# Kernel tuning notes

Hardware: AMD Instinct MI355X
Metric: run time of the kernel (lower is better)

## Reference

```python
import jax, jax.numpy as jnp
import numpy as np

RHO = 1.0
L = 50
RS = np.array([20, 40, 80, 160], dtype=np.int32)

def _get_index():
    S = []
    for m in range(-L // 2, L // 2 + 1):
        for n in range(-L // 2, L // 2 + 1):
            if abs(m * n) <= RHO * L // 2:
                S.append((m, n))
    return np.array(S, dtype=np.int32)

IDX = _get_index()          # [449, 2] (m, n) pairs
K = IDX.shape[0]            # 449
B, N, M = 8, 65536, 2       # batch, sequence length, Nmodes (dual-pol)


def setup_inputs() -> dict:
    key = jax.random.key(0)
    ks = jax.random.split(key, 8)
    shp = (B, N, M)
    inp = {
        "E_real": jax.random.normal(ks[0], shp, jnp.float32),
        "E_imag": jax.random.normal(ks[1], shp, jnp.float32),
        "F_real": jax.random.normal(ks[2], shp, jnp.float32),
        "F_imag": jax.random.normal(ks[3], shp, jnp.float32),
        "C1_real": jax.random.normal(ks[4], (len(RS), K), jnp.float32) * 0.01,
        "C1_imag": jax.random.normal(ks[5], (len(RS), K), jnp.float32) * 0.01,
        "C2_real": jax.random.normal(ks[6], (len(RS), K), jnp.float32) * 0.01,
        "C2_imag": jax.random.normal(ks[7], (len(RS), K), jnp.float32) * 0.01,
    }
    # task_info columns: (P [dBm], Fi, Fs [Hz], Nch); Fs must be 2e9 * some Rs entry
    ti = np.zeros((B, 4), dtype=np.float32)
    ti[:, 0] = 2.0
    ti[:, 2] = RS[np.arange(B) % len(RS)].astype(np.float32) * 2e9
    inp["task_info"] = jnp.asarray(ti)
    return inp


def _forward(E_real, E_imag, F_real, F_imag, C1_real, C1_imag, C2_real, C2_imag, task_info):
    E = E_real + 1j * E_imag    # [B, N, M] complex64
    F = F_real + 1j * F_imag

    # choose_C: map Fs -> row of C tables (sorted-Rs order, as in the torch code)
    rs_sorted = jnp.sort(jnp.asarray(RS))
    x = (task_info[:, 2] / 2e9).astype(jnp.int32)              # [B]
    ind = jnp.argmax(x[:, None] == rs_sorted[None, :], axis=-1)  # [B]
    C1 = (C1_real + 1j * C1_imag)[ind]                         # [B, K]
    C2 = (C2_real + 1j * C2_imag)[ind]                         # [B, K]

    ms = jnp.asarray(IDX[:, 0])
    ns = jnp.asarray(IDX[:, 1])

    def step(acc, xs):
        m, n, c1, c2 = xs                                       # c1, c2: [B]
        En  = jnp.roll(E, n, axis=-2)
        Em  = jnp.roll(E, m, axis=-2)
        Emn = jnp.roll(E, m + n, axis=-2)
        Fn  = jnp.roll(F, n, axis=-2)
        Fmn = jnp.roll(F, m + n, axis=-2)
        A = En * jnp.conj(Fmn) * c1[:, None, None] + Fn * jnp.conj(Emn) * c2[:, None, None]
        # (A + A.roll(1, dim=-1)) swaps/combines the two polarizations
        return acc + (A + jnp.roll(A, 1, axis=-1)) * Em, None

    acc, _ = jax.lax.scan(step, jnp.zeros_like(E), (ms, ns, C1.T, C2.T))

    P = jnp.power(10.0, task_info[:, 0] / 10.0) / E.shape[-1]   # [B]
    Eo = F + (jnp.sqrt(P) ** 3)[:, None, None] * acc
    return E[:, L:-L, :], Eo[:, L:-L, :]


def reference(E_real, E_imag, F_real, F_imag, C1_real, C1_imag, C2_real, C2_imag, task_info):
    return _forward(E_real, E_imag, F_real, F_imag,
                    C1_real, C1_imag, C2_real, C2_imag, task_info)
```

## Files before the change

### kernel.cpp

```cpp
#include <hip/hip_runtime.h>
#include <hip/hip_bf16.h>


namespace {

constexpr int NSEQ    = 65536;
constexpr int BATCH   = 8;
constexpr int KTAPS   = 449;
constexpr int NM      = 25;
constexpr int THREADS = 256;
constexpr int TILE    = 512;
constexpr int WIN     = TILE + 4 * NM;
constexpr int GHW     = TILE + 2 * NM;
constexpr int GHH     = (GHW + 1) / 2;

typedef float v2f __attribute__((ext_vector_type(2)));

__device__ inline v2f pkfma(float s, v2f v, v2f acc) {
  return __builtin_elementwise_fma((v2f){s, s}, v, acc);
}

__device__ inline void mac(v2f& U13, v2f& U42, v2f& V13, v2f& V42,
                           const float4 c, const float4 g) {
  const v2f glo = (v2f){g.x, g.y}, ghi = (v2f){g.z, g.w};
  U13 = pkfma(c.x, glo, U13); U42 = pkfma(c.y, glo, U42);
  V13 = pkfma(c.z, ghi, V13); V42 = pkfma(c.w, ghi, V42);
}

__device__ inline unsigned short f2bf(float f) {
  __hip_bfloat16 h = __float2bfloat16(f);
  union { __hip_bfloat16 hh; unsigned short u; } cv;
  cv.hh = h;
  return cv.u;
}

__global__ void prep_c_kernel(const float* __restrict__ c1r, const float* __restrict__ c1i,
                              const float* __restrict__ c2r, const float* __restrict__ c2i,
                              float4* __restrict__ cw) {
  int idx = blockIdx.x * blockDim.x + threadIdx.x;
  if (idx < 4 * KTAPS) cw[idx] = make_float4(c1r[idx], c1i[idx], c2r[idx], c2i[idx]);
}

__device__ inline float4 gh_entry(const float4 e, const float4 f,
                                  const float4 fm, const float4 em) {
  v2f G = (v2f){fm.w * e.w, fm.w * (-e.z)};
  G = pkfma(fm.x, (v2f){e.x, e.y}, G);
  G = pkfma(fm.y, (v2f){e.y, -e.x}, G);
  G = pkfma(fm.z, (v2f){e.z, e.w}, G);
  v2f H = (v2f){em.w * f.w, em.w * (-f.z)};
  H = pkfma(em.x, (v2f){f.x, f.y}, H);
  H = pkfma(em.y, (v2f){f.y, -f.x}, H);
  H = pkfma(em.z, (v2f){f.z, f.w}, H);
  return make_float4(G.x, G.y, H.x, H.y);
}

__global__ __launch_bounds__(THREADS, 4) void hpbc_kernel(
    const float2* __restrict__ er, const float2* __restrict__ ei,
    const float2* __restrict__ fr, const float2* __restrict__ fi,
    const float*  __restrict__ task, const float4* __restrict__ cw,
    unsigned short* __restrict__ out, int nout, int lpad, int ntiles)
{
  __shared__ float4 sE[WIN];
  __shared__ float4 sF[WIN];
  __shared__ float4 ghE[2][GHH];
  __shared__ float4 ghO[2][GHH];

  const int bx   = blockIdx.x;
  const int b    = bx / ntiles;
  const int tile = bx - b * ntiles;
  const int tid  = threadIdx.x;
  const int i0   = lpad + tile * TILE;
  const int elo  = i0 - 2 * NM;

  const float2* erb = er + (size_t)b * NSEQ;
  const float2* eib = ei + (size_t)b * NSEQ;
  const float2* frb = fr + (size_t)b * NSEQ;
  const float2* fib = fi + (size_t)b * NSEQ;

  for (int u = tid; u < WIN; u += THREADS) {
    int g = (elo + u) & (NSEQ - 1);
    float2 a = erb[g], c = eib[g];
    sE[u] = make_float4(a.x, c.x, a.y, c.y);
    float2 d = frb[g], e = fib[g];
    sF[u] = make_float4(d.x, e.x, d.y, e.y);
  }

  const float dbm = task[b * 4 + 0];
  const float fsr = task[b * 4 + 2];
  const int   x   = (int)(fsr / 2.0e9f);
  const int ind = (x == 40) ? 1 : (x == 80) ? 2 : (x == 160) ? 3 : 0;
  const float4* __restrict__ crow = cw + ind * KTAPS;
  const float P  = powf(10.0f, dbm * 0.1f) * 0.5f;
  const float pf = P * sqrtf(P);

  __syncthreads();

  const float4 e0 = sE[tid + NM],            f0 = sF[tid + NM];
  const float4 e1 = sE[tid + THREADS + NM],  f1 = sF[tid + THREADS + NM];
  const bool  has3 = (tid < GHW - 2 * THREADS);
  float4 e2 = make_float4(0,0,0,0), f2 = e2;
  if (has3) { e2 = sE[tid + 2*THREADS + NM]; f2 = sF[tid + 2*THREADS + NM]; }

  v2f A0 = {0,0}, A1 = {0,0}, B0 = {0,0}, B1 = {0,0};
  int kbase = 0, p = 0;
  float4 ebCarry = sE[2*tid + 1 + 2*NM + NM];

  for (int mm = -NM; mm <= NM; ++mm) {
    {
      const int s = NM - mm;
      const float4 g0 = gh_entry(e0, f0, sF[tid + s], sE[tid + s]);
      if (tid & 1) ghO[p][tid >> 1] = g0; else ghE[p][tid >> 1] = g0;
      const float4 g1 = gh_entry(e1, f1, sF[tid + THREADS + s], sE[tid + THREADS + s]);
      if (tid & 1) ghO[p][(tid + THREADS) >> 1] = g1; else ghE[p][(tid + THREADS) >> 1] = g1;
      if (has3) {
        const float4 g2 = gh_entry(e2, f2, sF[tid + 2*THREADS + s], sE[tid + 2*THREADS + s]);
        if (tid & 1) ghO[p][(tid + 2*THREADS) >> 1] = g2; else ghE[p][(tid + 2*THREADS) >> 1] = g2;
      }
    }
    __syncthreads();

    const int am   = mm < 0 ? -mm : mm;
    const int nmax = (mm == 0) ? NM : (NM / am);
    const int q    = nmax & 1;
    const float4* __restrict__ hiArr = q ? ghO[p] : ghE[p];
    const float4* __restrict__ loArr = q ? ghE[p] : ghO[p];
    const int h0 = tid + ((26 + nmax) >> 1);
    const int h1 = tid + ((25 + nmax) >> 1);

    v2f aU13={0,0}, aU42={0,0}, aV13={0,0}, aV42={0,0};
    v2f bU13={0,0}, bU42={0,0}, bV13={0,0}, bV42={0,0};
    float4 cOdd;
    {
      const float4 hi = hiArr[h0], lo = loArr[h1];
      const float4 c0 = crow[kbase], c1 = crow[kbase + 1];
      mac(bU13, bU42, bV13, bV42, c0, hi);
      mac(bU13, bU42, bV13, bV42, c1, lo);
      mac(aU13, aU42, aV13, aV42, c0, lo);
      cOdd = c1;
    }
    for (int s = 1; s < nmax; ++s) {
      const float4 hi = hiArr[h0 - s], lo = loArr[h1 - s];
      const float4 c2 = crow[kbase + 2*s], c3 = crow[kbase + 2*s + 1];
      mac(bU13, bU42, bV13, bV42, c2, hi);
      mac(bU13, bU42, bV13, bV42, c3, lo);
      mac(aU13, aU42, aV13, aV42, cOdd, hi);
      mac(aU13, aU42, aV13, aV42, c2, lo);
      cOdd = c3;
    }
    {
      const float4 hi = hiArr[h0 - nmax], lo = loArr[h1 - nmax];
      const float4 c2 = crow[kbase + 2*nmax];
      mac(bU13, bU42, bV13, bV42, c2, hi);
      mac(aU13, aU42, aV13, aV42, cOdd, hi);
      mac(aU13, aU42, aV13, aV42, c2, lo);
    }
    kbase += 2 * nmax + 1;

    const float sra = aU13.x - aU42.y + aV13.x - aV42.y;
    const float sia = aU13.y + aU42.x + aV13.y + aV42.x;
    const float srb = bU13.x - bU42.y + bV13.x - bV42.y;
    const float sib = bU13.y + bU42.x + bV13.y + bV42.x;

    const float4 ea = sE[2*tid + 2*NM - mm];
    const float4 eb = ebCarry;
    ebCarry = ea;
    A0 = pkfma(sra, (v2f){ea.x, ea.y}, pkfma(sia, (v2f){-ea.y, ea.x}, A0));
    A1 = pkfma(sra, (v2f){ea.z, ea.w}, pkfma(sia, (v2f){-ea.w, ea.z}, A1));
    B0 = pkfma(srb, (v2f){eb.x, eb.y}, pkfma(sib, (v2f){-eb.y, eb.x}, B0));
    B1 = pkfma(srb, (v2f){eb.z, eb.w}, pkfma(sib, (v2f){-eb.w, eb.z}, B1));
    p ^= 1;
  }

  const int end = lpad + nout;
  const size_t chunk1 = (size_t)BATCH * nout * 4;
  const int i = i0 + 2 * tid;
  if (i + 1 < end) {
    const float4 evA = sE[2*tid + 2*NM],     fvA = sF[2*tid + 2*NM];
    const float4 evB = sE[2*tid + 1 + 2*NM], fvB = sF[2*tid + 1 + 2*NM];
    const size_t o = ((size_t)b * nout + (size_t)(i - lpad)) * 4;
    ushort4 w0a, w0b, w1a, w1b;
    w0a.x = f2bf(evA.y); w0a.y = f2bf(evA.x); w0a.z = f2bf(evA.w); w0a.w = f2bf(evA.z);
    w0b.x = f2bf(evB.y); w0b.y = f2bf(evB.x); w0b.z = f2bf(evB.w); w0b.w = f2bf(evB.z);
    w1a.x = f2bf(fvA.y + pf * A0.y); w1a.y = f2bf(fvA.x + pf * A0.x);
    w1a.z = f2bf(fvA.w + pf * A1.y); w1a.w = f2bf(fvA.z + pf * A1.x);
    w1b.x = f2bf(fvB.y + pf * B0.y); w1b.y = f2bf(fvB.x + pf * B0.x);
    w1b.z = f2bf(fvB.w + pf * B1.y); w1b.w = f2bf(fvB.z + pf * B1.x);
    *reinterpret_cast<ushort4*>(out + o) = w0a;
    *reinterpret_cast<ushort4*>(out + o + 4) = w0b;
    *reinterpret_cast<ushort4*>(out + chunk1 + o) = w1a;
    *reinterpret_cast<ushort4*>(out + chunk1 + o + 4) = w1b;
  } else if (i < end) {
    const float4 evA = sE[2*tid + 2*NM], fvA = sF[2*tid + 2*NM];
    const size_t o = ((size_t)b * nout + (size_t)(i - lpad)) * 4;
    ushort4 w0a, w1a;
    w0a.x = f2bf(evA.y); w0a.y = f2bf(evA.x); w0a.z = f2bf(evA.w); w0a.w = f2bf(evA.z);
    w1a.x = f2bf(fvA.y + pf * A0.y); w1a.y = f2bf(fvA.x + pf * A0.x);
    w1a.z = f2bf(fvA.w + pf * A1.y); w1a.w = f2bf(fvA.z + pf * A1.x);
    *reinterpret_cast<ushort4*>(out + o) = w0a;
    *reinterpret_cast<ushort4*>(out + chunk1 + o) = w1a;
  }
}

}

extern "C" void kernel_launch(void* const* d_in, const int* in_sizes, int n_in,
                              void* d_out, int out_size, void* d_ws, size_t ws_size,
                              hipStream_t stream) {
  const float* E_real  = (const float*)d_in[0];
  const float* E_imag  = (const float*)d_in[1];
  const float* F_real  = (const float*)d_in[2];
  const float* F_imag  = (const float*)d_in[3];
  const float* C1_real = (const float*)d_in[4];
  const float* C1_imag = (const float*)d_in[5];
  const float* C2_real = (const float*)d_in[6];
  const float* C2_imag = (const float*)d_in[7];
  const float* task    = (const float*)d_in[8];

  int nout = out_size / 32;
  if (nout < 1 || nout > NSEQ) nout = NSEQ - 100;
  const int lpad   = (NSEQ - nout) / 2;
  const int ntiles = (nout + TILE - 1) / TILE;

  unsigned short* outp = (unsigned short*)d_out;
  float4* cw = (float4*)d_ws;

  hipLaunchKernelGGL(prep_c_kernel, dim3((4 * KTAPS + 255) / 256), dim3(256), 0, stream,
                     C1_real, C1_imag, C2_real, C2_imag, cw);

  hipLaunchKernelGGL(hpbc_kernel, dim3(BATCH * ntiles), dim3(THREADS), 0, stream,
                     (const float2*)E_real, (const float2*)E_imag,
                     (const float2*)F_real, (const float2*)F_imag,
                     task, cw, outp, nout, lpad, ntiles);
}
```

Before: 96.33 us.

## Fully unroll FIR inner loop per tap count and overlap next GH build with current FIR

```diff
diff --git a/kernel.cpp b/kernel.cpp
--- a/kernel.cpp
+++ b/kernel.cpp
@@ -54,6 +54,44 @@
   return make_float4(G.x, G.y, H.x, H.y);
 }
 
+template<int NMAX>
+__device__ inline void fir_unrolled(const float4* __restrict__ hiArr,
+                                    const float4* __restrict__ loArr,
+                                    const float4* __restrict__ cc,
+                                    int tid,
+                                    v2f& aU13, v2f& aU42, v2f& aV13, v2f& aV42,
+                                    v2f& bU13, v2f& bU42, v2f& bV13, v2f& bV42)
+{
+  const int h0 = tid + ((26 + NMAX) >> 1);
+  const int h1 = tid + ((25 + NMAX) >> 1);
+  float4 cOdd;
+  {
+    const float4 hi = hiArr[h0], lo = loArr[h1];
+    const float4 c0 = cc[0], c1 = cc[1];
+    mac(bU13, bU42, bV13, bV42, c0, hi);
+    mac(bU13, bU42, bV13, bV42, c1, lo);
+    mac(aU13, aU42, aV13, aV42, c0, lo);
+    cOdd = c1;
+  }
+#pragma unroll
+  for (int s = 1; s < NMAX; ++s) {
+    const float4 hi = hiArr[h0 - s], lo = loArr[h1 - s];
+    const float4 c2 = cc[2*s], c3 = cc[2*s + 1];
+    mac(bU13, bU42, bV13, bV42, c2, hi);
+    mac(bU13, bU42, bV13, bV42, c3, lo);
+    mac(aU13, aU42, aV13, aV42, cOdd, hi);
+    mac(aU13, aU42, aV13, aV42, c2, lo);
+    cOdd = c3;
+  }
+  {
+    const float4 hi = hiArr[h0 - NMAX], lo = loArr[h1 - NMAX];
+    const float4 c2 = cc[2*NMAX];
+    mac(bU13, bU42, bV13, bV42, c2, hi);
+    mac(aU13, aU42, aV13, aV42, cOdd, hi);
+    mac(aU13, aU42, aV13, aV42, c2, lo);
+  }
+}
+
 __global__ __launch_bounds__(THREADS, 4) void hpbc_kernel(
     const float2* __restrict__ er, const float2* __restrict__ ei,
     const float2* __restrict__ fr, const float2* __restrict__ fi,
@@ -62,8 +100,8 @@
 {
   __shared__ float4 sE[WIN];
   __shared__ float4 sF[WIN];
-  __shared__ float4 ghE[2][GHH];
-  __shared__ float4 ghO[2][GHH];
+  __shared__ float4 ghE0[GHH], ghO0[GHH];
+  __shared__ float4 ghE1[GHH], ghO1[GHH];
 
   const int bx   = blockIdx.x;
   const int b    = bx / ntiles;
@@ -102,59 +140,46 @@
   if (has3) { e2 = sE[tid + 2*THREADS + NM]; f2 = sF[tid + 2*THREADS + NM]; }
 
   v2f A0 = {0,0}, A1 = {0,0}, B0 = {0,0}, B1 = {0,0};
-  int kbase = 0, p = 0;
+  int kbase = 0;
   float4 ebCarry = sE[2*tid + 1 + 2*NM + NM];
 
-  for (int mm = -NM; mm <= NM; ++mm) {
-    {
-      const int s = NM - mm;
-      const float4 g0 = gh_entry(e0, f0, sF[tid + s], sE[tid + s]);
-      if (tid & 1) ghO[p][tid >> 1] = g0; else ghE[p][tid >> 1] = g0;
-      const float4 g1 = gh_entry(e1, f1, sF[tid + THREADS + s], sE[tid + THREADS + s]);
-      if (tid & 1) ghO[p][(tid + THREADS) >> 1] = g1; else ghE[p][(tid + THREADS) >> 1] = g1;
-      if (has3) {
-        const float4 g2 = gh_entry(e2, f2, sF[tid + 2*THREADS + s], sE[tid + 2*THREADS + s]);
-        if (tid & 1) ghO[p][(tid + 2*THREADS) >> 1] = g2; else ghE[p][(tid + 2*THREADS) >> 1] = g2;
-      }
+  auto write_gh = [&](float4* wE, float4* wO, int mmNext) {
+    const int s = NM - mmNext;
+    const float4 g0 = gh_entry(e0, f0, sF[tid + s], sE[tid + s]);
+    if (tid & 1) wO[tid >> 1] = g0; else wE[tid >> 1] = g0;
+    const float4 g1 = gh_entry(e1, f1, sF[tid + THREADS + s], sE[tid + THREADS + s]);
+    if (tid & 1) wO[(tid + THREADS) >> 1] = g1; else wE[(tid + THREADS) >> 1] = g1;
+    if (has3) {
+      const float4 g2 = gh_entry(e2, f2, sF[tid + 2*THREADS + s], sE[tid + 2*THREADS + s]);
+      if (tid & 1) wO[(tid + 2*THREADS) >> 1] = g2; else wE[(tid + 2*THREADS) >> 1] = g2;
     }
-    __syncthreads();
-
+  };
+
+  auto iter = [&](const float4* rE, const float4* rO,
+                  float4* wE, float4* wO, int mm) {
     const int am   = mm < 0 ? -mm : mm;
     const int nmax = (mm == 0) ? NM : (NM / am);
     const int q    = nmax & 1;
-    const float4* __restrict__ hiArr = q ? ghO[p] : ghE[p];
-    const float4* __restrict__ loArr = q ? ghE[p] : ghO[p];
-    const int h0 = tid + ((26 + nmax) >> 1);
-    const int h1 = tid + ((25 + nmax) >> 1);
+    const float4* hiArr = q ? rO : rE;
+    const float4* loArr = q ? rE : rO;
+    const float4* cc = crow + kbase;
 
     v2f aU13={0,0}, aU42={0,0}, aV13={0,0}, aV42={0,0};
     v2f bU13={0,0}, bU42={0,0}, bV13={0,0}, bV42={0,0};
-    float4 cOdd;
-    {
-      const float4 hi = hiArr[h0], lo = loArr[h1];
-      const float4 c0 = crow[kbase], c1 = crow[kbase + 1];
-      mac(bU13, bU42, bV13, bV42, c0, hi);
-      mac(bU13, bU42, bV13, bV42, c1, lo);
-      mac(aU13, aU42, aV13, aV42, c0, lo);
-      cOdd = c1;
-    }
-    for (int s = 1; s < nmax; ++s) {
-      const float4 hi = hiArr[h0 - s], lo = loArr[h1 - s];
-      const float4 c2 = crow[kbase + 2*s], c3 = crow[kbase + 2*s + 1];
-      mac(bU13, bU42, bV13, bV42, c2, hi);
-      mac(bU13, bU42, bV13, bV42, c3, lo);
-      mac(aU13, aU42, aV13, aV42, cOdd, hi);
-      mac(aU13, aU42, aV13, aV42, c2, lo);
-      cOdd = c3;
-    }
-    {
-      const float4 hi = hiArr[h0 - nmax], lo = loArr[h1 - nmax];
-      const float4 c2 = crow[kbase + 2*nmax];
-      mac(bU13, bU42, bV13, bV42, c2, hi);
-      mac(aU13, aU42, aV13, aV42, cOdd, hi);
-      mac(aU13, aU42, aV13, aV42, c2, lo);
+    switch (nmax) {
+      case 25: fir_unrolled<25>(hiArr, loArr, cc, tid, aU13,aU42,aV13,aV42, bU13,bU42,bV13,bV42); break;
+      case 12: fir_unrolled<12>(hiArr, loArr, cc, tid, aU13,aU42,aV13,aV42, bU13,bU42,bV13,bV42); break;
+      case  8: fir_unrolled< 8>(hiArr, loArr, cc, tid, aU13,aU42,aV13,aV42, bU13,bU42,bV13,bV42); break;
+      case  6: fir_unrolled< 6>(hiArr, loArr, cc, tid, aU13,aU42,aV13,aV42, bU13,bU42,bV13,bV42); break;
+      case  5: fir_unrolled< 5>(hiArr, loArr, cc, tid, aU13,aU42,aV13,aV42, bU13,bU42,bV13,bV42); break;
+      case  4: fir_unrolled< 4>(hiArr, loArr, cc, tid, aU13,aU42,aV13,aV42, bU13,bU42,bV13,bV42); break;
+      case  3: fir_unrolled< 3>(hiArr, loArr, cc, tid, aU13,aU42,aV13,aV42, bU13,bU42,bV13,bV42); break;
+      case  2: fir_unrolled< 2>(hiArr, loArr, cc, tid, aU13,aU42,aV13,aV42, bU13,bU42,bV13,bV42); break;
+      default: fir_unrolled< 1>(hiArr, loArr, cc, tid, aU13,aU42,aV13,aV42, bU13,bU42,bV13,bV42); break;
     }
     kbase += 2 * nmax + 1;
+
+    if (mm < NM) write_gh(wE, wO, mm + 1);
 
     const float sra = aU13.x - aU42.y + aV13.x - aV42.y;
     const float sia = aU13.y + aU42.x + aV13.y + aV42.x;
@@ -168,7 +193,17 @@
     A1 = pkfma(sra, (v2f){ea.z, ea.w}, pkfma(sia, (v2f){-ea.w, ea.z}, A1));
     B0 = pkfma(srb, (v2f){eb.x, eb.y}, pkfma(sib, (v2f){-eb.y, eb.x}, B0));
     B1 = pkfma(srb, (v2f){eb.z, eb.w}, pkfma(sib, (v2f){-eb.w, eb.z}, B1));
-    p ^= 1;
+
+    __syncthreads();
+  };
+
+  write_gh(ghE0, ghO0, -NM);
+  __syncthreads();
+
+  for (int mm = -NM; mm <= NM; mm += 2) {
+    iter(ghE0, ghO0, ghE1, ghO1, mm);
+    if (mm + 1 <= NM)
+      iter(ghE1, ghO1, ghE0, ghO0, mm + 1);
   }
 
   const int end = lpad + nout;
```

Measured after the change: 88.32 us. -8.3%, faster.
